# Kernel optimization log

Hardware: AMD Instinct MI355X
Metric: run time of the kernel (lower is better)

Reference implementation:

```python
import jax, jax.numpy as jnp
import numpy as np

BATCH = 8192          # per-modality batch size; n = 2*BATCH
FEAT = 128            # feature dim (kept small -> memory-bound n^2 distance matrix)
NUM_IDS = 1000
MARGIN = 0.3


def setup_inputs() -> dict:
    key = jax.random.key(0)
    k1, k2 = jax.random.split(key)
    n = 2 * BATCH
    inputs = jax.random.normal(k1, (n, FEAT), dtype=jnp.float32)
    # same identity set in both modality halves -> cross-modal positives exist per row
    t = jax.random.randint(k2, (BATCH,), 0, NUM_IDS, dtype=jnp.int32)
    targets = jnp.concatenate([t, t], axis=0)
    return {"inputs": inputs, "targets": targets}


def reference(inputs, targets):
    n = inputs.shape[0]
    # pairwise euclidean distances: ||xi||^2 + ||xj||^2 - 2 xi.xj
    sq = jnp.sum(inputs * inputs, axis=1)                      # [n]
    d2 = sq[:, None] + sq[None, :] - 2.0 * (inputs @ inputs.T)  # [n, n]
    dist = jnp.sqrt(jnp.clip(d2, 1e-12, None))
    # modality: first half 0, second half 1; self.sub selects CROSS-modality pairs
    modality = jnp.arange(n) >= (n // 2)
    cross = modality[:, None] != modality[None, :]              # [n, n] bool
    same = targets[:, None] == targets[None, :]                 # same identity
    pos = same & cross        # mask1: same label, different modality
    neg = (~same) & cross     # mask2: diff label, different modality
    # masked hard mining: per-row max over positives, min over negatives
    dist_ap = jnp.max(jnp.where(pos, dist, -jnp.inf), axis=1)   # [n]
    dist_an = jnp.min(jnp.where(neg, dist, jnp.inf), axis=1)    # [n]
    # MarginRankingLoss with y=1: mean(relu(-(dist_an - dist_ap) + margin))
    loss = jnp.mean(jax.nn.relu(dist_ap - dist_an + MARGIN))
    correct = jnp.sum(dist_an >= dist_ap).astype(jnp.int32)
    return (loss, correct)
```

## Files before the change

kernel.cpp:

```cpp
#include <hip/hip_runtime.h>

#define N_TOTAL 16384
#define HALF    8192
#define FEAT    128
#define MARGIN  0.3f
#define NBINS   1024

typedef __attribute__((ext_vector_type(8))) short  short8v;
typedef __attribute__((ext_vector_type(4))) float  float4v;

__device__ __forceinline__ unsigned short f32_to_bf16_rne(float f) {
    unsigned u = __float_as_uint(f);
    u += 0x7FFFu + ((u >> 16) & 1u);
    return (unsigned short)(u >> 16);
}

__global__ __launch_bounds__(256) void hist_kernel(
        const int* __restrict__ targets, int* __restrict__ hist) {
    int i = blockIdx.x * 256 + threadIdx.x;
    int h = i >> 13;
    atomicAdd(&hist[(h << 10) + targets[i]], 1);
}

__global__ __launch_bounds__(1024) void scan_kernel(
        const int* __restrict__ hist, int* __restrict__ cursor) {
    const int h = blockIdx.x;
    const int t = threadIdx.x;
    const int lane = t & 63, wave = t >> 6;
    int x = hist[(h << 10) + t];
    const int orig = x;
    #pragma unroll
    for (int m = 1; m < 64; m <<= 1) {
        int v = __shfl_up(x, m, 64);
        if (lane >= m) x += v;
    }
    __shared__ int wsum[16], woff[16];
    if (lane == 63) wsum[wave] = x;
    __syncthreads();
    if (t == 0) {
        int s = 0;
        for (int w = 0; w < 16; ++w) { woff[w] = s; s += wsum[w]; }
    }
    __syncthreads();
    cursor[(h << 10) + t] = x + woff[wave] - orig;
}

__global__ __launch_bounds__(256) void scatter_kernel(
        const int* __restrict__ targets, int* __restrict__ cursor,
        int* __restrict__ perm, int* __restrict__ labs) {
    int i = blockIdx.x * 256 + threadIdx.x;
    int h = i >> 13;
    int lbl = targets[i];
    int pos = atomicAdd(&cursor[(h << 10) + lbl], 1);
    int dst = (h << 13) + pos;
    perm[dst] = i;
    labs[dst] = lbl;
}

__global__ __launch_bounds__(256) void prep_kernel(
        const float* __restrict__ X, const int* __restrict__ perm,
        unsigned* __restrict__ Xb, float* __restrict__ sq,
        int* __restrict__ maxpos, int* __restrict__ minneg) {
    const int wave = threadIdx.x >> 6, lane = threadIdx.x & 63;
    const int r = blockIdx.x * 4 + wave;
    const int src = perm[r];
    const float2 xv = ((const float2*)(X + (size_t)src * FEAT))[lane];
    unsigned short h0 = f32_to_bf16_rne(xv.x);
    unsigned short h1 = f32_to_bf16_rne(xv.y);
    Xb[r * 64 + lane] = (unsigned)h0 | ((unsigned)h1 << 16);
    float x0 = __uint_as_float((unsigned)h0 << 16);
    float x1 = __uint_as_float((unsigned)h1 << 16);
    float p = x0 * x0 + x1 * x1;
    #pragma unroll
    for (int m = 1; m < 64; m <<= 1) p += __shfl_xor(p, m, 64);
    if (lane == 0) {
        sq[r] = p;
        maxpos[r] = (int)0xFF800000u;
        minneg[r] = 0x7F800000;
    }
}

__global__ __launch_bounds__(256, 2) void cross_kernel(
        const unsigned short* __restrict__ Xb, const float* __restrict__ sq,
        const int* __restrict__ labs,
        int* __restrict__ maxpos, int* __restrict__ minneg) {
    __shared__ unsigned short As[128 * 128];
    __shared__ unsigned short Bs[128 * 128];
    const int bm = blockIdx.x, bn = blockIdx.y;
    const int t  = threadIdx.x;

    const unsigned short* Ag = Xb + (size_t)bm * 128 * FEAT;
    const unsigned short* Bg = Xb + (size_t)(HALF + bn * 128) * FEAT;
    #pragma unroll
    for (int p = 0; p < 8; ++p) {
        int idx = p * 256 + t;
        int row = idx >> 4, ch = idx & 15;
        int sc  = ch ^ (row & 7);
        uint4 va = ((const uint4*)Ag)[idx];
        uint4 vb = ((const uint4*)Bg)[idx];
        *(uint4*)&As[row * 128 + sc * 8] = va;
        *(uint4*)&Bs[row * 128 + sc * 8] = vb;
    }
    __syncthreads();

    const int wave = t >> 6, lane = t & 63;
    const int q = lane >> 4, c = lane & 15;
    const int wr = (wave >> 1) * 64, wc = (wave & 1) * 64;

    float4v acc[4][4] = {};
    #pragma unroll
    for (int kk = 0; kk < 4; ++kk) {
        short8v af[4], bfr[4];
        #pragma unroll
        for (int ti = 0; ti < 4; ++ti) {
            int row = wr + ti * 16 + c;
            int sc  = (kk * 4 + q) ^ (row & 7);
            af[ti] = *(const short8v*)&As[row * 128 + sc * 8];
        }
        #pragma unroll
        for (int tj = 0; tj < 4; ++tj) {
            int row = wc + tj * 16 + c;
            int sc  = (kk * 4 + q) ^ (row & 7);
            bfr[tj] = *(const short8v*)&Bs[row * 128 + sc * 8];
        }
        #pragma unroll
        for (int ti = 0; ti < 4; ++ti)
            #pragma unroll
            for (int tj = 0; tj < 4; ++tj)
                acc[ti][tj] = __builtin_amdgcn_mfma_f32_16x16x32_bf16(
                    af[ti], bfr[tj], acc[ti][tj], 0, 0, 0);
    }

    const float NEG_INF = __int_as_float((int)0xFF800000u);
    const float POS_INF = __int_as_float(0x7F800000);

    const int aMin = labs[bm * 128], aMax = labs[bm * 128 + 127];
    const int bMn  = labs[HALF + bn * 128], bMx = labs[HALF + bn * 128 + 127];
    const bool overlap = (aMax >= bMn) && (bMx >= aMin);

    float sA[16];
    #pragma unroll
    for (int ti = 0; ti < 4; ++ti)
        #pragma unroll
        for (int reg = 0; reg < 4; ++reg)
            sA[ti * 4 + reg] = sq[bm * 128 + wr + ti * 16 + q * 4 + reg];
    float sB[4];
    #pragma unroll
    for (int tj = 0; tj < 4; ++tj)
        sB[tj] = sq[HALF + bn * 128 + wc + tj * 16 + c];

    float rmin[16], cmin[4];
    #pragma unroll
    for (int i = 0; i < 16; ++i) rmin[i] = POS_INF;
    #pragma unroll
    for (int j = 0; j < 4; ++j)  cmin[j] = POS_INF;

    if (!overlap) {
        #pragma unroll
        for (int ti = 0; ti < 4; ++ti)
            #pragma unroll
            for (int tj = 0; tj < 4; ++tj)
                #pragma unroll
                for (int reg = 0; reg < 4; ++reg) {
                    int ri = ti * 4 + reg;
                    float d2 = fmaf(acc[ti][tj][reg], -2.0f, sA[ri] + sB[tj]);
                    rmin[ri] = fminf(rmin[ri], d2);
                    cmin[tj] = fminf(cmin[tj], d2);
                }
        #pragma unroll
        for (int m = 1; m <= 8; m <<= 1)
            #pragma unroll
            for (int i = 0; i < 16; ++i)
                rmin[i] = fminf(rmin[i], __shfl_xor(rmin[i], m, 64));
        if (c == 0) {
            #pragma unroll
            for (int ti = 0; ti < 4; ++ti)
                #pragma unroll
                for (int reg = 0; reg < 4; ++reg)
                    atomicMin(&minneg[bm * 128 + wr + ti * 16 + q * 4 + reg],
                              __float_as_int(rmin[ti * 4 + reg]));
        }
        #pragma unroll
        for (int m = 16; m <= 32; m <<= 1)
            #pragma unroll
            for (int j = 0; j < 4; ++j)
                cmin[j] = fminf(cmin[j], __shfl_xor(cmin[j], m, 64));
        if (q == 0) {
            #pragma unroll
            for (int tj = 0; tj < 4; ++tj)
                atomicMin(&minneg[HALF + bn * 128 + wc + tj * 16 + c],
                          __float_as_int(cmin[tj]));
        }
    } else {
        float rmax[16], cmax[4];
        #pragma unroll
        for (int i = 0; i < 16; ++i) rmax[i] = NEG_INF;
        #pragma unroll
        for (int j = 0; j < 4; ++j)  cmax[j] = NEG_INF;

        int tA[16];
        #pragma unroll
        for (int ti = 0; ti < 4; ++ti)
            #pragma unroll
            for (int reg = 0; reg < 4; ++reg)
                tA[ti * 4 + reg] = labs[bm * 128 + wr + ti * 16 + q * 4 + reg];
        int tB[4];
        #pragma unroll
        for (int tj = 0; tj < 4; ++tj)
            tB[tj] = labs[HALF + bn * 128 + wc + tj * 16 + c];

        #pragma unroll
        for (int ti = 0; ti < 4; ++ti)
            #pragma unroll
            for (int tj = 0; tj < 4; ++tj) {
                #pragma unroll
                for (int reg = 0; reg < 4; ++reg) {
                    int ri = ti * 4 + reg;
                    float d2 = fmaf(acc[ti][tj][reg], -2.0f, sA[ri] + sB[tj]);
                    bool same = (tA[ri] == tB[tj]);
                    float posc = same ? d2 : NEG_INF;
                    float negc = same ? POS_INF : d2;
                    rmax[ri] = fmaxf(rmax[ri], posc);
                    cmax[tj] = fmaxf(cmax[tj], posc);
                    rmin[ri] = fminf(rmin[ri], negc);
                    cmin[tj] = fminf(cmin[tj], negc);
                }
            }
        #pragma unroll
        for (int m = 1; m <= 8; m <<= 1)
            #pragma unroll
            for (int i = 0; i < 16; ++i) {
                rmax[i] = fmaxf(rmax[i], __shfl_xor(rmax[i], m, 64));
                rmin[i] = fminf(rmin[i], __shfl_xor(rmin[i], m, 64));
            }
        if (c == 0) {
            #pragma unroll
            for (int ti = 0; ti < 4; ++ti)
                #pragma unroll
                for (int reg = 0; reg < 4; ++reg) {
                    int gi = bm * 128 + wr + ti * 16 + q * 4 + reg;
                    atomicMax(&maxpos[gi], __float_as_int(rmax[ti * 4 + reg]));
                    atomicMin(&minneg[gi], __float_as_int(rmin[ti * 4 + reg]));
                }
        }
        #pragma unroll
        for (int m = 16; m <= 32; m <<= 1)
            #pragma unroll
            for (int j = 0; j < 4; ++j) {
                cmax[j] = fmaxf(cmax[j], __shfl_xor(cmax[j], m, 64));
                cmin[j] = fminf(cmin[j], __shfl_xor(cmin[j], m, 64));
            }
        if (q == 0) {
            #pragma unroll
            for (int tj = 0; tj < 4; ++tj) {
                int gj = HALF + bn * 128 + wc + tj * 16 + c;
                atomicMax(&maxpos[gj], __float_as_int(cmax[tj]));
                atomicMin(&minneg[gj], __float_as_int(cmin[tj]));
            }
        }
    }
}

__global__ __launch_bounds__(256) void final_kernel(
        const int* __restrict__ maxpos, const int* __restrict__ minneg,
        float* __restrict__ accF, int* __restrict__ accI) {
    const int i = blockIdx.x * 256 + threadIdx.x;
    const int t = threadIdx.x;
    float ap = sqrtf(fmaxf(__int_as_float(maxpos[i]), 1e-12f));
    float an = sqrtf(fmaxf(__int_as_float(minneg[i]), 1e-12f));
    float term = fmaxf(ap - an + MARGIN, 0.0f);
    int cnt = (an >= ap) ? 1 : 0;
    #pragma unroll
    for (int m = 1; m < 64; m <<= 1) {
        term += __shfl_xor(term, m, 64);
        cnt  += __shfl_xor(cnt, m, 64);
    }
    __shared__ float sf[4];
    __shared__ int   si[4];
    if ((t & 63) == 0) { sf[t >> 6] = term; si[t >> 6] = cnt; }
    __syncthreads();
    if (t == 0) {
        atomicAdd(accF, sf[0] + sf[1] + sf[2] + sf[3]);
        atomicAdd(accI, si[0] + si[1] + si[2] + si[3]);
    }
}

__global__ void write_kernel(const float* __restrict__ accF,
                             const int* __restrict__ accI,
                             float* __restrict__ out) {
    out[0] = *accF / (float)N_TOTAL;
    out[1] = (float)(*accI);
}

extern "C" void kernel_launch(void* const* d_in, const int* in_sizes, int n_in,
                              void* d_out, int out_size, void* d_ws, size_t ws_size,
                              hipStream_t stream) {
    const float* X       = (const float*)d_in[0];
    const int*   targets = (const int*)d_in[1];
    float* out = (float*)d_out;

    char* ws = (char*)d_ws;
    const size_t XB_BYTES = (size_t)N_TOTAL * FEAT * 2;
    unsigned* Xb  = (unsigned*)ws;
    float* sq     = (float*)(ws + XB_BYTES);
    int* maxpos   = (int*)(ws + XB_BYTES + 1 * 65536);
    int* minneg   = (int*)(ws + XB_BYTES + 2 * 65536);
    int* perm     = (int*)(ws + XB_BYTES + 3 * 65536);
    int* labs     = (int*)(ws + XB_BYTES + 4 * 65536);
    int* hist     = (int*)(ws + XB_BYTES + 5 * 65536);
    int* cursor   = hist + 2 * NBINS;
    float* accF   = (float*)(cursor + 2 * NBINS);
    int*   accI   = (int*)(accF + 1);

    hipMemsetAsync(hist, 0, 4 * NBINS * sizeof(int) + 8, stream);

    hist_kernel   <<<64, 256, 0, stream>>>(targets, hist);
    scan_kernel   <<<2, 1024, 0, stream>>>(hist, cursor);
    scatter_kernel<<<64, 256, 0, stream>>>(targets, cursor, perm, labs);
    prep_kernel   <<<4096, 256, 0, stream>>>(X, perm, Xb, sq, maxpos, minneg);
    cross_kernel  <<<dim3(64, 64), 256, 0, stream>>>(
        (const unsigned short*)Xb, sq, labs, maxpos, minneg);
    final_kernel  <<<64, 256, 0, stream>>>(maxpos, minneg, accF, accI);
    write_kernel  <<<1, 1, 0, stream>>>(accF, accI, out);
}
```

Before: 131.1 us.

## Merge sort prologue kernels, fuse scatter into prep, widen cross blocks to 512 threads

The separate histogram, scan and scatter kernels and the memset are replaced by one single-block shared-memory counting-sort kernel. The scatter atomics now happen inside prep_kernel, which writes bf16 rows, norms and labels directly to their sorted slots. The write kernel is folded into final_kernel through a last-block ticket counter. Separately, cross_kernel runs 512 threads per 128x128 tile, with each wave owning a 32x64 sub-tile instead of 64x64, to reduce per-thread registers and raise wave occupancy. This cuts several launches but serialises the histogram on one block and halves register-level reuse in the MFMA tile.

Result: no change. 132.7 us (+1.3%).

```diff
diff --git a/kernel.cpp b/kernel.cpp
--- a/kernel.cpp
+++ b/kernel.cpp
@@ -15,72 +15,75 @@
     return (unsigned short)(u >> 16);
 }
 
-__global__ __launch_bounds__(256) void hist_kernel(
-        const int* __restrict__ targets, int* __restrict__ hist) {
-    int i = blockIdx.x * 256 + threadIdx.x;
-    int h = i >> 13;
-    atomicAdd(&hist[(h << 10) + targets[i]], 1);
-}
-
-__global__ __launch_bounds__(1024) void scan_kernel(
-        const int* __restrict__ hist, int* __restrict__ cursor) {
-    const int h = blockIdx.x;
+__global__ __launch_bounds__(1024) void sort_init_kernel(
+        const int* __restrict__ targets, int* __restrict__ cursor,
+        int* __restrict__ accs ) {
+    __shared__ int lhist[2 * NBINS];
     const int t = threadIdx.x;
+    lhist[t] = 0; lhist[NBINS + t] = 0;
+    __syncthreads();
+    #pragma unroll
+    for (int k = 0; k < 16; ++k) {
+        int i = k * 1024 + t;
+        int h = i >> 13;
+        atomicAdd(&lhist[(h << 10) + targets[i]], 1);
+    }
+    __syncthreads();
     const int lane = t & 63, wave = t >> 6;
-    int x = hist[(h << 10) + t];
-    const int orig = x;
+    int x0 = lhist[t], x1 = lhist[NBINS + t];
+    const int o0 = x0, o1 = x1;
     #pragma unroll
     for (int m = 1; m < 64; m <<= 1) {
-        int v = __shfl_up(x, m, 64);
-        if (lane >= m) x += v;
-    }
-    __shared__ int wsum[16], woff[16];
-    if (lane == 63) wsum[wave] = x;
+        int v0 = __shfl_up(x0, m, 64);
+        int v1 = __shfl_up(x1, m, 64);
+        if (lane >= m) { x0 += v0; x1 += v1; }
+    }
+    __shared__ int wsum[32];
+    if (lane == 63) { wsum[wave] = x0; wsum[16 + wave] = x1; }
     __syncthreads();
     if (t == 0) {
         int s = 0;
-        for (int w = 0; w < 16; ++w) { woff[w] = s; s += wsum[w]; }
-    }
-    __syncthreads();
-    cursor[(h << 10) + t] = x + woff[wave] - orig;
-}
-
-__global__ __launch_bounds__(256) void scatter_kernel(
-        const int* __restrict__ targets, int* __restrict__ cursor,
-        int* __restrict__ perm, int* __restrict__ labs) {
-    int i = blockIdx.x * 256 + threadIdx.x;
-    int h = i >> 13;
-    int lbl = targets[i];
-    int pos = atomicAdd(&cursor[(h << 10) + lbl], 1);
-    int dst = (h << 13) + pos;
-    perm[dst] = i;
-    labs[dst] = lbl;
+        for (int w = 0; w < 16; ++w)  { int v = wsum[w]; wsum[w] = s; s += v; }
+        s = 0;
+        for (int w = 16; w < 32; ++w) { int v = wsum[w]; wsum[w] = s; s += v; }
+        accs[0] = 0; accs[1] = 0; accs[2] = 0;
+    }
+    __syncthreads();
+    cursor[t]         = x0 - o0 + wsum[wave];
+    cursor[NBINS + t] = x1 - o1 + wsum[16 + wave];
 }
 
 __global__ __launch_bounds__(256) void prep_kernel(
-        const float* __restrict__ X, const int* __restrict__ perm,
-        unsigned* __restrict__ Xb, float* __restrict__ sq,
+        const float* __restrict__ X, const int* __restrict__ targets,
+        int* __restrict__ cursor,
+        unsigned* __restrict__ Xb, float* __restrict__ sq, int* __restrict__ labs,
         int* __restrict__ maxpos, int* __restrict__ minneg) {
     const int wave = threadIdx.x >> 6, lane = threadIdx.x & 63;
-    const int r = blockIdx.x * 4 + wave;
-    const int src = perm[r];
+    const int src = blockIdx.x * 4 + wave;
+    const int h   = src >> 13;
+    const int lbl = targets[src];
+    int dst;
+    if (lane == 0)
+        dst = (h << 13) + atomicAdd(&cursor[(h << 10) + lbl], 1);
+    dst = __shfl(dst, 0, 64);
     const float2 xv = ((const float2*)(X + (size_t)src * FEAT))[lane];
     unsigned short h0 = f32_to_bf16_rne(xv.x);
     unsigned short h1 = f32_to_bf16_rne(xv.y);
-    Xb[r * 64 + lane] = (unsigned)h0 | ((unsigned)h1 << 16);
+    Xb[dst * 64 + lane] = (unsigned)h0 | ((unsigned)h1 << 16);
     float x0 = __uint_as_float((unsigned)h0 << 16);
     float x1 = __uint_as_float((unsigned)h1 << 16);
     float p = x0 * x0 + x1 * x1;
     #pragma unroll
     for (int m = 1; m < 64; m <<= 1) p += __shfl_xor(p, m, 64);
     if (lane == 0) {
-        sq[r] = p;
-        maxpos[r] = (int)0xFF800000u;
-        minneg[r] = 0x7F800000;
-    }
-}
-
-__global__ __launch_bounds__(256, 2) void cross_kernel(
+        sq[dst]     = p;
+        labs[dst]   = lbl;
+        maxpos[dst] = (int)0xFF800000u;
+        minneg[dst] = 0x7F800000;
+    }
+}
+
+__global__ __launch_bounds__(512, 4) void cross_kernel(
         const unsigned short* __restrict__ Xb, const float* __restrict__ sq,
         const int* __restrict__ labs,
         int* __restrict__ maxpos, int* __restrict__ minneg) {
@@ -92,8 +95,8 @@
     const unsigned short* Ag = Xb + (size_t)bm * 128 * FEAT;
     const unsigned short* Bg = Xb + (size_t)(HALF + bn * 128) * FEAT;
     #pragma unroll
-    for (int p = 0; p < 8; ++p) {
-        int idx = p * 256 + t;
+    for (int p = 0; p < 4; ++p) {
+        int idx = p * 512 + t;
         int row = idx >> 4, ch = idx & 15;
         int sc  = ch ^ (row & 7);
         uint4 va = ((const uint4*)Ag)[idx];
@@ -105,14 +108,15 @@
 
     const int wave = t >> 6, lane = t & 63;
     const int q = lane >> 4, c = lane & 15;
-    const int wr = (wave >> 1) * 64, wc = (wave & 1) * 64;
-
-    float4v acc[4][4] = {};
+    const int wr = (wave >> 1) * 32;
+    const int wc = (wave & 1) * 64;
+
+    float4v acc[2][4] = {};
     #pragma unroll
     for (int kk = 0; kk < 4; ++kk) {
-        short8v af[4], bfr[4];
-        #pragma unroll
-        for (int ti = 0; ti < 4; ++ti) {
+        short8v af[2], bfr[4];
+        #pragma unroll
+        for (int ti = 0; ti < 2; ++ti) {
             int row = wr + ti * 16 + c;
             int sc  = (kk * 4 + q) ^ (row & 7);
             af[ti] = *(const short8v*)&As[row * 128 + sc * 8];
@@ -124,7 +128,7 @@
             bfr[tj] = *(const short8v*)&Bs[row * 128 + sc * 8];
         }
         #pragma unroll
-        for (int ti = 0; ti < 4; ++ti)
+        for (int ti = 0; ti < 2; ++ti)
             #pragma unroll
             for (int tj = 0; tj < 4; ++tj)
                 acc[ti][tj] = __builtin_amdgcn_mfma_f32_16x16x32_bf16(
@@ -138,9 +142,9 @@
     const int bMn  = labs[HALF + bn * 128], bMx = labs[HALF + bn * 128 + 127];
     const bool overlap = (aMax >= bMn) && (bMx >= aMin);
 
-    float sA[16];
-    #pragma unroll
-    for (int ti = 0; ti < 4; ++ti)
+    float sA[8];
+    #pragma unroll
+    for (int ti = 0; ti < 2; ++ti)
         #pragma unroll
         for (int reg = 0; reg < 4; ++reg)
             sA[ti * 4 + reg] = sq[bm * 128 + wr + ti * 16 + q * 4 + reg];
@@ -149,15 +153,15 @@
     for (int tj = 0; tj < 4; ++tj)
         sB[tj] = sq[HALF + bn * 128 + wc + tj * 16 + c];
 
-    float rmin[16], cmin[4];
-    #pragma unroll
-    for (int i = 0; i < 16; ++i) rmin[i] = POS_INF;
-    #pragma unroll
-    for (int j = 0; j < 4; ++j)  cmin[j] = POS_INF;
+    float rmin[8], cmin[4];
+    #pragma unroll
+    for (int i = 0; i < 8; ++i) rmin[i] = POS_INF;
+    #pragma unroll
+    for (int j = 0; j < 4; ++j) cmin[j] = POS_INF;
 
     if (!overlap) {
         #pragma unroll
-        for (int ti = 0; ti < 4; ++ti)
+        for (int ti = 0; ti < 2; ++ti)
             #pragma unroll
             for (int tj = 0; tj < 4; ++tj)
                 #pragma unroll
@@ -170,11 +174,11 @@
         #pragma unroll
         for (int m = 1; m <= 8; m <<= 1)
             #pragma unroll
-            for (int i = 0; i < 16; ++i)
+            for (int i = 0; i < 8; ++i)
                 rmin[i] = fminf(rmin[i], __shfl_xor(rmin[i], m, 64));
         if (c == 0) {
             #pragma unroll
-            for (int ti = 0; ti < 4; ++ti)
+            for (int ti = 0; ti < 2; ++ti)
                 #pragma unroll
                 for (int reg = 0; reg < 4; ++reg)
                     atomicMin(&minneg[bm * 128 + wr + ti * 16 + q * 4 + reg],
@@ -192,15 +196,15 @@
                           __float_as_int(cmin[tj]));
         }
     } else {
-        float rmax[16], cmax[4];
-        #pragma unroll
-        for (int i = 0; i < 16; ++i) rmax[i] = NEG_INF;
-        #pragma unroll
-        for (int j = 0; j < 4; ++j)  cmax[j] = NEG_INF;
-
-        int tA[16];
-        #pragma unroll
-        for (int ti = 0; ti < 4; ++ti)
+        float rmax[8], cmax[4];
+        #pragma unroll
+        for (int i = 0; i < 8; ++i) rmax[i] = NEG_INF;
+        #pragma unroll
+        for (int j = 0; j < 4; ++j) cmax[j] = NEG_INF;
+
+        int tA[8];
+        #pragma unroll
+        for (int ti = 0; ti < 2; ++ti)
             #pragma unroll
             for (int reg = 0; reg < 4; ++reg)
                 tA[ti * 4 + reg] = labs[bm * 128 + wr + ti * 16 + q * 4 + reg];
@@ -210,7 +214,7 @@
             tB[tj] = labs[HALF + bn * 128 + wc + tj * 16 + c];
 
         #pragma unroll
-        for (int ti = 0; ti < 4; ++ti)
+        for (int ti = 0; ti < 2; ++ti)
             #pragma unroll
             for (int tj = 0; tj < 4; ++tj) {
                 #pragma unroll
@@ -229,13 +233,13 @@
         #pragma unroll
         for (int m = 1; m <= 8; m <<= 1)
             #pragma unroll
-            for (int i = 0; i < 16; ++i) {
+            for (int i = 0; i < 8; ++i) {
                 rmax[i] = fmaxf(rmax[i], __shfl_xor(rmax[i], m, 64));
                 rmin[i] = fminf(rmin[i], __shfl_xor(rmin[i], m, 64));
             }
         if (c == 0) {
             #pragma unroll
-            for (int ti = 0; ti < 4; ++ti)
+            for (int ti = 0; ti < 2; ++ti)
                 #pragma unroll
                 for (int reg = 0; reg < 4; ++reg) {
                     int gi = bm * 128 + wr + ti * 16 + q * 4 + reg;
@@ -263,9 +267,13 @@
 
 __global__ __launch_bounds__(256) void final_kernel(
         const int* __restrict__ maxpos, const int* __restrict__ minneg,
-        float* __restrict__ accF, int* __restrict__ accI) {
+        int* __restrict__ accs ,
+        float* __restrict__ out) {
     const int i = blockIdx.x * 256 + threadIdx.x;
     const int t = threadIdx.x;
+    float* accF  = (float*)&accs[0];
+    int*   accI  = &accs[1];
+    int*   tick  = &accs[2];
     float ap = sqrtf(fmaxf(__int_as_float(maxpos[i]), 1e-12f));
     float an = sqrtf(fmaxf(__int_as_float(minneg[i]), 1e-12f));
     float term = fmaxf(ap - an + MARGIN, 0.0f);
@@ -282,14 +290,16 @@
     if (t == 0) {
         atomicAdd(accF, sf[0] + sf[1] + sf[2] + sf[3]);
         atomicAdd(accI, si[0] + si[1] + si[2] + si[3]);
-    }
-}
-
-__global__ void write_kernel(const float* __restrict__ accF,
-                             const int* __restrict__ accI,
-                             float* __restrict__ out) {
-    out[0] = *accF / (float)N_TOTAL;
-    out[1] = (float)(*accI);
+        __threadfence();
+        int old = atomicAdd(tick, 1);
+        if (old == gridDim.x - 1) {
+            __threadfence();
+            float S = atomicAdd(accF, 0.0f);
+            int   C = atomicAdd(accI, 0);
+            out[0] = S / (float)N_TOTAL;
+            out[1] = (float)C;
+        }
+    }
 }
 
 extern "C" void kernel_launch(void* const* d_in, const int* in_sizes, int n_in,
@@ -305,21 +315,14 @@
     float* sq     = (float*)(ws + XB_BYTES);
     int* maxpos   = (int*)(ws + XB_BYTES + 1 * 65536);
     int* minneg   = (int*)(ws + XB_BYTES + 2 * 65536);
-    int* perm     = (int*)(ws + XB_BYTES + 3 * 65536);
-    int* labs     = (int*)(ws + XB_BYTES + 4 * 65536);
-    int* hist     = (int*)(ws + XB_BYTES + 5 * 65536);
-    int* cursor   = hist + 2 * NBINS;
-    float* accF   = (float*)(cursor + 2 * NBINS);
-    int*   accI   = (int*)(accF + 1);
-
-    hipMemsetAsync(hist, 0, 4 * NBINS * sizeof(int) + 8, stream);
-
-    hist_kernel   <<<64, 256, 0, stream>>>(targets, hist);
-    scan_kernel   <<<2, 1024, 0, stream>>>(hist, cursor);
-    scatter_kernel<<<64, 256, 0, stream>>>(targets, cursor, perm, labs);
-    prep_kernel   <<<4096, 256, 0, stream>>>(X, perm, Xb, sq, maxpos, minneg);
-    cross_kernel  <<<dim3(64, 64), 256, 0, stream>>>(
+    int* labs     = (int*)(ws + XB_BYTES + 3 * 65536);
+    int* cursor   = (int*)(ws + XB_BYTES + 4 * 65536);
+    int* accs     = cursor + 2 * NBINS;
+
+    sort_init_kernel<<<1, 1024, 0, stream>>>(targets, cursor, accs);
+    prep_kernel     <<<4096, 256, 0, stream>>>(X, targets, cursor, Xb, sq, labs,
+                                               maxpos, minneg);
+    cross_kernel    <<<dim3(64, 64), 512, 0, stream>>>(
         (const unsigned short*)Xb, sq, labs, maxpos, minneg);
-    final_kernel  <<<64, 256, 0, stream>>>(maxpos, minneg, accF, accI);
-    write_kernel  <<<1, 1, 0, stream>>>(accF, accI, out);
-}
+    final_kernel    <<<64, 256, 0, stream>>>(maxpos, minneg, accs, out);
+}
```
